# Optimization experiments

Measured on AMD Instinct MI355X. Metric: run time of the kernel, lower is better.

## Reference

```python
import jax, jax.numpy as jnp
import numpy as np


def setup_inputs() -> dict:
    key = jax.random.key(0)
    ks = jax.random.split(key, 6)
    S, B, E = 2048, 2, 1024
    scale = 1.0 / np.sqrt(E)
    return {
        "query": jax.random.normal(ks[0], (S, B, E), dtype=jnp.float32),
        "key": jax.random.normal(ks[1], (S, B, E), dtype=jnp.float32),
        "value": jax.random.normal(ks[2], (S, B, E), dtype=jnp.float32),
        "in_proj_w": jax.random.normal(ks[3], (3 * E, E), dtype=jnp.float32) * scale,
        "in_proj_b": jnp.zeros((3 * E,), dtype=jnp.float32),
        "out_proj_w": jax.random.normal(ks[4], (E, E), dtype=jnp.float32) * scale,
        "out_proj_b": jnp.zeros((E,), dtype=jnp.float32),
        "num_heads": 16,
        "block_size": 128,
    }


def reference(query, key, value, in_proj_w, in_proj_b, out_proj_w, out_proj_b,
              num_heads, block_size):
    # Shapes: query/key/value [S, B, E] (torch MHA default, batch_first=False)
    S, B, E = query.shape
    H = num_heads
    D = E // H

    wq, wk, wv = jnp.split(in_proj_w, 3, axis=0)   # each [E, E]
    bq, bk, bv = jnp.split(in_proj_b, 3, axis=0)   # each [E]

    def proj(x, w, b):
        # [S,B,E] @ [E,E]^T + b -> [B,H,S,D]
        y = x @ w.T + b
        return y.reshape(S, B, H, D).transpose(1, 2, 0, 3)

    q = proj(query, wq, bq) * (1.0 / np.sqrt(D))
    k = proj(key, wk, bk)
    v = proj(value, wv, bv)

    # Dense scores with banded mask: allowed iff i-block <= j <= i+block-1
    scores = jnp.einsum("bhsd,bhtd->bhst", q, k)  # [B,H,S,S]
    i = jnp.arange(S)[:, None]
    j = jnp.arange(S)[None, :]
    allowed = (j >= i - block_size) & (j < i + block_size)  # [S,S]
    neg_inf = jnp.asarray(-jnp.inf, dtype=scores.dtype)
    scores = jnp.where(allowed[None, None], scores, neg_inf)

    attn = jax.nn.softmax(scores, axis=-1)
    ctx = jnp.einsum("bhst,bhtd->bhsd", attn, v)           # [B,H,S,D]
    ctx = ctx.transpose(2, 0, 1, 3).reshape(S, B, E)       # [S,B,E]
    return ctx @ out_proj_w.T + out_proj_b
```

## Files before the change

### kernel.cpp

```cpp
#include <hip/hip_runtime.h>
#include <hip/hip_bf16.h>

#define S_LEN 2048
#define BATCH 2
#define EMB   1024
#define NHEAD 16
#define HDIM  64
#define WIN   128

typedef __attribute__((ext_vector_type(8))) short short8;
typedef __attribute__((ext_vector_type(4))) float floatx4;

__device__ __forceinline__ unsigned int pk2bf(float a, float b) {
    unsigned int ua = __builtin_bit_cast(unsigned int, a);
    unsigned int ub = __builtin_bit_cast(unsigned int, b);
    ua += 0x7fffu + ((ua >> 16) & 1u);
    ub += 0x7fffu + ((ub >> 16) & 1u);
    return (ua >> 16) | (ub & 0xffff0000u);
}
__device__ __forceinline__ unsigned short f2bf(float f) {
    unsigned int u = __builtin_bit_cast(unsigned int, f);
    u += 0x7fffu + ((u >> 16) & 1u);
    return (unsigned short)(u >> 16);
}

__device__ __forceinline__ void gl_lds16(const unsigned short* g, unsigned short* l) {
    __builtin_amdgcn_global_load_lds(
        (const __attribute__((address_space(1))) unsigned int*)g,
        (__attribute__((address_space(3))) unsigned int*)l,
        16, 0, 0);
}

#define QKV_UNITS 524288
#define WI_UNITS  393216
#define WO_UNITS  131072

__global__ __launch_bounds__(256)
void convert_kernel(const float* __restrict__ xq, const float* __restrict__ xk,
                    const float* __restrict__ xv, const float* __restrict__ wi,
                    const float* __restrict__ wo,
                    unsigned short* __restrict__ xqb, unsigned short* __restrict__ xkb,
                    unsigned short* __restrict__ xvb, unsigned short* __restrict__ wib,
                    unsigned short* __restrict__ wob)
{
    const size_t u = (size_t)blockIdx.x * 256 + threadIdx.x;
    const float* src;
    unsigned short* dst;
    size_t off;
    if (u < 3 * (size_t)QKV_UNITS) {
        const int which = (int)(u / QKV_UNITS);
        off = (u % QKV_UNITS) * 8;
        src = (which == 0) ? xq : (which == 1) ? xk : xv;
        dst = (which == 0) ? xqb : (which == 1) ? xkb : xvb;
    } else if (u < 3 * (size_t)QKV_UNITS + WI_UNITS) {
        off = (u - 3 * (size_t)QKV_UNITS) * 8;
        src = wi; dst = wib;
    } else {
        off = (u - (3 * (size_t)QKV_UNITS + WI_UNITS)) * 8;
        src = wo; dst = wob;
    }
    float4 a = *reinterpret_cast<const float4*>(src + off);
    float4 b = *reinterpret_cast<const float4*>(src + off + 4);
    uint4 p = {pk2bf(a.x, a.y), pk2bf(a.z, a.w), pk2bf(b.x, b.y), pk2bf(b.z, b.w)};
    *reinterpret_cast<uint4*>(dst + off) = p;
}

__global__ __launch_bounds__(256)
void qkv_gemm_kernel(const unsigned short* __restrict__ xqb,
                     const unsigned short* __restrict__ xkb,
                     const unsigned short* __restrict__ xvb,
                     const unsigned short* __restrict__ wib,
                     const float* __restrict__ bias,
                     unsigned short* __restrict__ qo,
                     unsigned short* __restrict__ ko,
                     unsigned short* __restrict__ vto)
{
    __shared__ unsigned short As[128 * 32];
    __shared__ unsigned short Bs[128 * 32];

    const int bid  = blockIdx.x;
    const int which = bid >> 8;
    const int bx   = (bid >> 5) & 7;
    const int by   = bid & 31;

    const unsigned short* A = (which == 0) ? xqb : (which == 1) ? xkb : xvb;
    const unsigned short* W = wib + (size_t)which * EMB * EMB;
    const float* bv = bias + which * EMB;
    const float scale = (which == 0) ? 0.125f : 1.0f;

    const int tid  = threadIdx.x;
    const int lane = tid & 63;
    const int wave = tid >> 6;
    const int quad = lane >> 4;
    const int c16  = lane & 15;
    const int wm   = (wave & 1) << 6;
    const int wn   = (wave >> 1) << 6;

    const int rowBase = by * 128;
    const int colBase = bx * 128;

    const int lrow = lane >> 2;
    const int lseg = (((lane & 3) ^ (lrow & 3)) << 3);

    floatx4 acc[4][4];
    #pragma unroll
    for (int i = 0; i < 4; ++i)
        #pragma unroll
        for (int j = 0; j < 4; ++j)
            acc[i][j] = (floatx4){0.f, 0.f, 0.f, 0.f};

    const int rxor = c16 & 3;

    for (int k0 = 0; k0 < EMB; k0 += 32) {
        __syncthreads();
        #pragma unroll
        for (int t = 0; t < 2; ++t) {
            const int c = wave * 2 + t;
            const int row = c * 16 + lrow;
            gl_lds16(A + (size_t)(rowBase + row) * EMB + k0 + lseg, &As[c * 512]);
            gl_lds16(W + (size_t)(colBase + row) * EMB + k0 + lseg, &Bs[c * 512]);
        }
        __syncthreads();

        const int soff = ((quad ^ rxor) << 3);
        short8 af[4], bf[4];
        #pragma unroll
        for (int mi = 0; mi < 4; ++mi)
            af[mi] = *reinterpret_cast<const short8*>(
                &As[(wm + mi * 16 + c16) * 32 + soff]);
        #pragma unroll
        for (int ni = 0; ni < 4; ++ni)
            bf[ni] = *reinterpret_cast<const short8*>(
                &Bs[(wn + ni * 16 + c16) * 32 + soff]);

        #pragma unroll
        for (int mi = 0; mi < 4; ++mi)
            #pragma unroll
            for (int ni = 0; ni < 4; ++ni)
                acc[mi][ni] = __builtin_amdgcn_mfma_f32_16x16x32_bf16(
                    af[mi], bf[ni], acc[mi][ni], 0, 0, 0);
    }

    #pragma unroll
    for (int ni = 0; ni < 4; ++ni) {
        const int n_full = colBase + wn + ni * 16 + c16;
        const float bb = bv[n_full];
        const int h = n_full >> 6;
        const int d = n_full & 63;
        #pragma unroll
        for (int mi = 0; mi < 4; ++mi) {
            #pragma unroll
            for (int r = 0; r < 4; ++r) {
                const int m_g = rowBase + wm + mi * 16 + quad * 4 + r;
                const int s   = m_g >> 1;
                const int b   = m_g & 1;
                const int bh  = b * NHEAD + h;
                const unsigned short val = f2bf((acc[mi][ni][r] + bb) * scale);
                if (which == 2)
                    vto[((size_t)bh * HDIM + d) * S_LEN + s] = val;
                else if (which == 0)
                    qo[((size_t)bh * S_LEN + s) * HDIM + d] = val;
                else
                    ko[((size_t)bh * S_LEN + s) * HDIM + d] = val;
            }
        }
    }
}

#define AT_STRIDE 72

__global__ __launch_bounds__(256)
void attn_mfma_kernel(const unsigned short* __restrict__ q,
                      const unsigned short* __restrict__ k,
                      const unsigned short* __restrict__ vt,
                      unsigned short* __restrict__ ctx)
{
    __shared__ unsigned short Qs[64 * AT_STRIDE];
    __shared__ unsigned short Ks[64 * AT_STRIDE];
    __shared__ unsigned short Vts[64 * AT_STRIDE];
    __shared__ unsigned short Ps[64 * AT_STRIDE];

    const int bid = blockIdx.x;
    const int bh  = bid & 31;
    const int s0  = (bid >> 5) * 64;
    const int tid = threadIdx.x;
    const int lane = tid & 63;
    const int wave = tid >> 6;
    const int quad = lane >> 4;
    const int c16  = lane & 15;

    const size_t base_qk = ((size_t)bh * S_LEN) * HDIM;
    const size_t base_vt = ((size_t)bh * HDIM) * S_LEN;

    const int srow = tid >> 2;
    const int sseg = (tid & 3) << 4;
    {
        const unsigned short* src = q + base_qk + (size_t)(s0 + srow) * HDIM + sseg;
        uint4 v0 = *reinterpret_cast<const uint4*>(src);
        uint4 v1 = *reinterpret_cast<const uint4*>(src + 8);
        *reinterpret_cast<uint4*>(&Qs[srow * AT_STRIDE + sseg])     = v0;
        *reinterpret_cast<uint4*>(&Qs[srow * AT_STRIDE + sseg + 8]) = v1;
    }

    float m_[4], l_[4];
    floatx4 ob[4];
    #pragma unroll
    for (int r = 0; r < 4; ++r) { m_[r] = -1.0e30f; l_[r] = 0.f; }
    #pragma unroll
    for (int dt = 0; dt < 4; ++dt) ob[dt] = (floatx4){0.f, 0.f, 0.f, 0.f};

    int c0 = s0 - 128; if (c0 < 0) c0 = 0;
    int c1 = s0 + 192; if (c1 > S_LEN) c1 = S_LEN;

    for (int cb = c0; cb < c1; cb += 64) {
        __syncthreads();
        {
            const unsigned short* ksrc = k + base_qk + (size_t)(cb + srow) * HDIM + sseg;
            const unsigned short* vsrc = vt + base_vt + (size_t)srow * S_LEN + cb + sseg;
            uint4 k0v = *reinterpret_cast<const uint4*>(ksrc);
            uint4 k1v = *reinterpret_cast<const uint4*>(ksrc + 8);
            uint4 v0v = *reinterpret_cast<const uint4*>(vsrc);
            uint4 v1v = *reinterpret_cast<const uint4*>(vsrc + 8);
            *reinterpret_cast<uint4*>(&Ks[srow * AT_STRIDE + sseg])      = k0v;
            *reinterpret_cast<uint4*>(&Ks[srow * AT_STRIDE + sseg + 8])  = k1v;
            *reinterpret_cast<uint4*>(&Vts[srow * AT_STRIDE + sseg])     = v0v;
            *reinterpret_cast<uint4*>(&Vts[srow * AT_STRIDE + sseg + 8]) = v1v;
        }
        __syncthreads();

        floatx4 sc[4];
        #pragma unroll
        for (int jt = 0; jt < 4; ++jt) sc[jt] = (floatx4){0.f, 0.f, 0.f, 0.f};
        {
            short8 af0 = *reinterpret_cast<const short8*>(
                &Qs[(wave * 16 + c16) * AT_STRIDE + quad * 8]);
            short8 af1 = *reinterpret_cast<const short8*>(
                &Qs[(wave * 16 + c16) * AT_STRIDE + 32 + quad * 8]);
            #pragma unroll
            for (int jt = 0; jt < 4; ++jt) {
                short8 bf0 = *reinterpret_cast<const short8*>(
                    &Ks[(jt * 16 + c16) * AT_STRIDE + quad * 8]);
                short8 bf1 = *reinterpret_cast<const short8*>(
                    &Ks[(jt * 16 + c16) * AT_STRIDE + 32 + quad * 8]);
                sc[jt] = __builtin_amdgcn_mfma_f32_16x16x32_bf16(af0, bf0, sc[jt], 0, 0, 0);
                sc[jt] = __builtin_amdgcn_mfma_f32_16x16x32_bf16(af1, bf1, sc[jt], 0, 0, 0);
            }
        }

        #pragma unroll
        for (int r = 0; r < 4; ++r) {
            const int qg = s0 + wave * 16 + quad * 4 + r;
            float rm = -3.0e38f;
            #pragma unroll
            for (int jt = 0; jt < 4; ++jt) {
                const int jg = cb + jt * 16 + c16;
                float x = sc[jt][r];
                if (jg < qg - WIN || jg >= qg + WIN) x = -3.0e38f;
                sc[jt][r] = x;
                rm = fmaxf(rm, x);
            }
            rm = fmaxf(rm, __shfl_xor(rm, 1));
            rm = fmaxf(rm, __shfl_xor(rm, 2));
            rm = fmaxf(rm, __shfl_xor(rm, 4));
            rm = fmaxf(rm, __shfl_xor(rm, 8));
            const float mn    = fmaxf(m_[r], rm);
            const float alpha = __expf(m_[r] - mn);
            float rs = 0.f;
            #pragma unroll
            for (int jt = 0; jt < 4; ++jt) {
                const float p = __expf(sc[jt][r] - mn);
                sc[jt][r] = p;
                rs += p;
            }
            rs += __shfl_xor(rs, 1);
            rs += __shfl_xor(rs, 2);
            rs += __shfl_xor(rs, 4);
            rs += __shfl_xor(rs, 8);
            l_[r] = l_[r] * alpha + rs;
            m_[r] = mn;
            #pragma unroll
            for (int dt = 0; dt < 4; ++dt) ob[dt][r] *= alpha;
        }

        #pragma unroll
        for (int jt = 0; jt < 4; ++jt)
            #pragma unroll
            for (int r = 0; r < 4; ++r)
                Ps[(wave * 16 + quad * 4 + r) * AT_STRIDE + jt * 16 + c16] =
                    f2bf(sc[jt][r]);

        {
            short8 pa0 = *reinterpret_cast<const short8*>(
                &Ps[(wave * 16 + c16) * AT_STRIDE + quad * 8]);
            short8 pa1 = *reinterpret_cast<const short8*>(
                &Ps[(wave * 16 + c16) * AT_STRIDE + 32 + quad * 8]);
            #pragma unroll
            for (int dt = 0; dt < 4; ++dt) {
                short8 bv0 = *reinterpret_cast<const short8*>(
                    &Vts[(dt * 16 + c16) * AT_STRIDE + quad * 8]);
                short8 bv1 = *reinterpret_cast<const short8*>(
                    &Vts[(dt * 16 + c16) * AT_STRIDE + 32 + quad * 8]);
                ob[dt] = __builtin_amdgcn_mfma_f32_16x16x32_bf16(pa0, bv0, ob[dt], 0, 0, 0);
                ob[dt] = __builtin_amdgcn_mfma_f32_16x16x32_bf16(pa1, bv1, ob[dt], 0, 0, 0);
            }
        }
    }

    const int b = bh >> 4;
    const int h = bh & 15;
    #pragma unroll
    for (int r = 0; r < 4; ++r) {
        const int sg  = s0 + wave * 16 + quad * 4 + r;
        const float inv = 1.0f / l_[r];
        #pragma unroll
        for (int dt = 0; dt < 4; ++dt) {
            const int d = dt * 16 + c16;
            ctx[((size_t)(sg * BATCH + b) << 10) + (h << 6) + d] = f2bf(ob[dt][r] * inv);
        }
    }
}

__global__ __launch_bounds__(256)
void out_gemm_kernel(const unsigned short* __restrict__ ctxb,
                     const unsigned short* __restrict__ wob,
                     const float* __restrict__ bias,
                     float* __restrict__ out)
{
    __shared__ unsigned short As[128 * 32];
    __shared__ unsigned short Bs[128 * 32];

    const int bid = blockIdx.x;
    const int bx  = bid >> 5;
    const int by  = bid & 31;

    const int tid  = threadIdx.x;
    const int lane = tid & 63;
    const int wave = tid >> 6;
    const int quad = lane >> 4;
    const int c16  = lane & 15;
    const int wm   = (wave & 1) << 6;
    const int wn   = (wave >> 1) << 6;

    const int rowBase = by * 128;
    const int colBase = bx * 128;

    const int lrow = lane >> 2;
    const int lseg = (((lane & 3) ^ (lrow & 3)) << 3);

    floatx4 acc[4][4];
    #pragma unroll
    for (int i = 0; i < 4; ++i)
        #pragma unroll
        for (int j = 0; j < 4; ++j)
            acc[i][j] = (floatx4){0.f, 0.f, 0.f, 0.f};

    const int rxor = c16 & 3;

    for (int k0 = 0; k0 < EMB; k0 += 32) {
        __syncthreads();
        #pragma unroll
        for (int t = 0; t < 2; ++t) {
            const int c = wave * 2 + t;
            const int row = c * 16 + lrow;
            gl_lds16(ctxb + (size_t)(rowBase + row) * EMB + k0 + lseg, &As[c * 512]);
            gl_lds16(wob  + (size_t)(colBase + row) * EMB + k0 + lseg, &Bs[c * 512]);
        }
        __syncthreads();

        const int soff = ((quad ^ rxor) << 3);
        short8 af[4], bf[4];
        #pragma unroll
        for (int mi = 0; mi < 4; ++mi)
            af[mi] = *reinterpret_cast<const short8*>(
                &As[(wm + mi * 16 + c16) * 32 + soff]);
        #pragma unroll
        for (int ni = 0; ni < 4; ++ni)
            bf[ni] = *reinterpret_cast<const short8*>(
                &Bs[(wn + ni * 16 + c16) * 32 + soff]);

        #pragma unroll
        for (int mi = 0; mi < 4; ++mi)
            #pragma unroll
            for (int ni = 0; ni < 4; ++ni)
                acc[mi][ni] = __builtin_amdgcn_mfma_f32_16x16x32_bf16(
                    af[mi], bf[ni], acc[mi][ni], 0, 0, 0);
    }

    #pragma unroll
    for (int ni = 0; ni < 4; ++ni) {
        const int n_full = colBase + wn + ni * 16 + c16;
        const float bb = bias[n_full];
        #pragma unroll
        for (int mi = 0; mi < 4; ++mi) {
            #pragma unroll
            for (int r = 0; r < 4; ++r) {
                const int m_g = rowBase + wm + mi * 16 + quad * 4 + r;
                out[(size_t)m_g * EMB + n_full] = acc[mi][ni][r] + bb;
            }
        }
    }
}

extern "C" void kernel_launch(void* const* d_in, const int* in_sizes, int n_in,
                              void* d_out, int out_size, void* d_ws, size_t ws_size,
                              hipStream_t stream) {
    const float* query = (const float*)d_in[0];
    const float* key   = (const float*)d_in[1];
    const float* value = (const float*)d_in[2];
    const float* in_w  = (const float*)d_in[3];
    const float* in_b  = (const float*)d_in[4];
    const float* out_w = (const float*)d_in[5];
    const float* out_b = (const float*)d_in[6];

    const size_t PLANE = (size_t)BATCH * NHEAD * S_LEN * HDIM;
    unsigned short* xqb = (unsigned short*)d_ws;
    unsigned short* xkb = xqb + PLANE;
    unsigned short* xvb = xkb + PLANE;
    unsigned short* wib = xvb + PLANE;
    unsigned short* wob = wib + (size_t)3 * EMB * EMB;
    unsigned short* qo  = wob + (size_t)EMB * EMB;
    unsigned short* ko  = qo + PLANE;
    unsigned short* vto = ko + PLANE;
    unsigned short* cw  = vto + PLANE;

    convert_kernel<<<8192, 256, 0, stream>>>(query, key, value, in_w, out_w,
                                             xqb, xkb, xvb, wib, wob);

    qkv_gemm_kernel<<<768, 256, 0, stream>>>(xqb, xkb, xvb, wib, in_b, qo, ko, vto);

    attn_mfma_kernel<<<1024, 256, 0, stream>>>(qo, ko, vto, cw);

    out_gemm_kernel<<<256, 256, 0, stream>>>(cw, wob, out_b, (float*)d_out);
}
```

Before: 201.5 us.

## Double-buffer GEMM LDS tiles, prefetch attention K/V, and stage V-transpose through LDS

Measured after the change: 214.7 us. 6.6% more time.

```diff
diff --git a/kernel.cpp b/kernel.cpp
--- a/kernel.cpp
+++ b/kernel.cpp
@@ -75,8 +75,8 @@
                      unsigned short* __restrict__ ko,
                      unsigned short* __restrict__ vto)
 {
-    __shared__ unsigned short As[128 * 32];
-    __shared__ unsigned short Bs[128 * 32];
+    __shared__ unsigned short As[2][128 * 32];
+    __shared__ unsigned short Bs[2][128 * 32];
 
     const int bid  = blockIdx.x;
     const int which = bid >> 8;
@@ -110,28 +110,37 @@
             acc[i][j] = (floatx4){0.f, 0.f, 0.f, 0.f};
 
     const int rxor = c16 & 3;
-
-    for (int k0 = 0; k0 < EMB; k0 += 32) {
-        __syncthreads();
-        #pragma unroll
-        for (int t = 0; t < 2; ++t) {
-            const int c = wave * 2 + t;
-            const int row = c * 16 + lrow;
-            gl_lds16(A + (size_t)(rowBase + row) * EMB + k0 + lseg, &As[c * 512]);
-            gl_lds16(W + (size_t)(colBase + row) * EMB + k0 + lseg, &Bs[c * 512]);
-        }
-        __syncthreads();
-
-        const int soff = ((quad ^ rxor) << 3);
+    const int soff = ((quad ^ rxor) << 3);
+
+#define STAGE_QKV(buf, kk)                                                        \
+    {                                                                             \
+        _Pragma("unroll")                                                         \
+        for (int t = 0; t < 2; ++t) {                                             \
+            const int c = wave * 2 + t;                                           \
+            const int row = c * 16 + lrow;                                        \
+            gl_lds16(A + (size_t)(rowBase + row) * EMB + (kk) + lseg,             \
+                     &As[buf][c * 512]);                                          \
+            gl_lds16(W + (size_t)(colBase + row) * EMB + (kk) + lseg,             \
+                     &Bs[buf][c * 512]);                                          \
+        }                                                                         \
+    }
+
+    STAGE_QKV(0, 0);
+    __syncthreads();
+
+    for (int it = 0; it < EMB / 32; ++it) {
+        const int cur = it & 1;
+        if (it + 1 < EMB / 32) STAGE_QKV(cur ^ 1, (it + 1) * 32);
+
         short8 af[4], bf[4];
         #pragma unroll
         for (int mi = 0; mi < 4; ++mi)
             af[mi] = *reinterpret_cast<const short8*>(
-                &As[(wm + mi * 16 + c16) * 32 + soff]);
+                &As[cur][(wm + mi * 16 + c16) * 32 + soff]);
         #pragma unroll
         for (int ni = 0; ni < 4; ++ni)
             bf[ni] = *reinterpret_cast<const short8*>(
-                &Bs[(wn + ni * 16 + c16) * 32 + soff]);
+                &Bs[cur][(wn + ni * 16 + c16) * 32 + soff]);
 
         #pragma unroll
         for (int mi = 0; mi < 4; ++mi)
@@ -139,30 +148,68 @@
             for (int ni = 0; ni < 4; ++ni)
                 acc[mi][ni] = __builtin_amdgcn_mfma_f32_16x16x32_bf16(
                     af[mi], bf[ni], acc[mi][ni], 0, 0, 0);
-    }
-
-    #pragma unroll
-    for (int ni = 0; ni < 4; ++ni) {
-        const int n_full = colBase + wn + ni * 16 + c16;
-        const float bb = bv[n_full];
+
+        __syncthreads();
+    }
+#undef STAGE_QKV
+
+    if (which != 2) {
+        #pragma unroll
+        for (int ni = 0; ni < 4; ++ni) {
+            const int n_full = colBase + wn + ni * 16 + c16;
+            const float bb = bv[n_full];
+            const int h = n_full >> 6;
+            const int d = n_full & 63;
+            #pragma unroll
+            for (int mi = 0; mi < 4; ++mi) {
+                #pragma unroll
+                for (int r = 0; r < 4; ++r) {
+                    const int m_g = rowBase + wm + mi * 16 + quad * 4 + r;
+                    const int s   = m_g >> 1;
+                    const int b   = m_g & 1;
+                    const int bh  = b * NHEAD + h;
+                    const unsigned short val = f2bf((acc[mi][ni][r] + bb) * scale);
+                    if (which == 0)
+                        qo[((size_t)bh * S_LEN + s) * HDIM + d] = val;
+                    else
+                        ko[((size_t)bh * S_LEN + s) * HDIM + d] = val;
+                }
+            }
+        }
+    } else {
+        unsigned short* Ts = (wn == 0) ? &As[0][0] : &Bs[0][0];
+        #pragma unroll
+        for (int ni = 0; ni < 4; ++ni) {
+            const int n_loc2 = ni * 16 + c16;
+            const int n_full = colBase + wn + n_loc2;
+            const float bb = bv[n_full];
+            const int k2 = (n_loc2 & 3) << 4;
+            #pragma unroll
+            for (int mi = 0; mi < 4; ++mi) {
+                #pragma unroll
+                for (int r = 0; r < 4; ++r) {
+                    const int m_local = wm + mi * 16 + quad * 4 + r;
+                    const int lin = (m_local & 1) * 64 + (m_local >> 1);
+                    Ts[n_loc2 * 128 + (lin ^ k2)] = f2bf(acc[mi][ni][r] + bb);
+                }
+            }
+        }
+        __syncthreads();
+        const int nl = tid & 127;
+        const int b  = tid >> 7;
+        const int n_loc2 = nl & 63;
+        const unsigned short* Tsrc = (nl < 64) ? &As[0][0] : &Bs[0][0];
+        const int k2 = (n_loc2 & 3) << 4;
+        const int n_full = colBase + nl;
         const int h = n_full >> 6;
         const int d = n_full & 63;
-        #pragma unroll
-        for (int mi = 0; mi < 4; ++mi) {
-            #pragma unroll
-            for (int r = 0; r < 4; ++r) {
-                const int m_g = rowBase + wm + mi * 16 + quad * 4 + r;
-                const int s   = m_g >> 1;
-                const int b   = m_g & 1;
-                const int bh  = b * NHEAD + h;
-                const unsigned short val = f2bf((acc[mi][ni][r] + bb) * scale);
-                if (which == 2)
-                    vto[((size_t)bh * HDIM + d) * S_LEN + s] = val;
-                else if (which == 0)
-                    qo[((size_t)bh * S_LEN + s) * HDIM + d] = val;
-                else
-                    ko[((size_t)bh * S_LEN + s) * HDIM + d] = val;
-            }
+        const int bh = b * NHEAD + h;
+        unsigned short* dst = vto + ((size_t)bh * HDIM + d) * S_LEN + (rowBase >> 1);
+        #pragma unroll
+        for (int g = 0; g < 8; ++g) {
+            const uint4 vv = *reinterpret_cast<const uint4*>(
+                &Tsrc[n_loc2 * 128 + ((b * 64 + g * 8) ^ k2)]);
+            *reinterpret_cast<uint4*>(dst + g * 8) = vv;
         }
     }
 }
@@ -212,21 +259,27 @@
     int c0 = s0 - 128; if (c0 < 0) c0 = 0;
     int c1 = s0 + 192; if (c1 > S_LEN) c1 = S_LEN;
 
+    uint4 k0v, k1v, v0v, v1v;
+#define LOADKV(CB)                                                                \
+    {                                                                             \
+        const unsigned short* ksrc = k + base_qk + (size_t)((CB) + srow) * HDIM + sseg; \
+        const unsigned short* vsrc = vt + base_vt + (size_t)srow * S_LEN + (CB) + sseg; \
+        k0v = *reinterpret_cast<const uint4*>(ksrc);                              \
+        k1v = *reinterpret_cast<const uint4*>(ksrc + 8);                          \
+        v0v = *reinterpret_cast<const uint4*>(vsrc);                              \
+        v1v = *reinterpret_cast<const uint4*>(vsrc + 8);                          \
+    }
+
+    LOADKV(c0);
+
     for (int cb = c0; cb < c1; cb += 64) {
         __syncthreads();
-        {
-            const unsigned short* ksrc = k + base_qk + (size_t)(cb + srow) * HDIM + sseg;
-            const unsigned short* vsrc = vt + base_vt + (size_t)srow * S_LEN + cb + sseg;
-            uint4 k0v = *reinterpret_cast<const uint4*>(ksrc);
-            uint4 k1v = *reinterpret_cast<const uint4*>(ksrc + 8);
-            uint4 v0v = *reinterpret_cast<const uint4*>(vsrc);
-            uint4 v1v = *reinterpret_cast<const uint4*>(vsrc + 8);
-            *reinterpret_cast<uint4*>(&Ks[srow * AT_STRIDE + sseg])      = k0v;
-            *reinterpret_cast<uint4*>(&Ks[srow * AT_STRIDE + sseg + 8])  = k1v;
-            *reinterpret_cast<uint4*>(&Vts[srow * AT_STRIDE + sseg])     = v0v;
-            *reinterpret_cast<uint4*>(&Vts[srow * AT_STRIDE + sseg + 8]) = v1v;
-        }
+        *reinterpret_cast<uint4*>(&Ks[srow * AT_STRIDE + sseg])      = k0v;
+        *reinterpret_cast<uint4*>(&Ks[srow * AT_STRIDE + sseg + 8])  = k1v;
+        *reinterpret_cast<uint4*>(&Vts[srow * AT_STRIDE + sseg])     = v0v;
+        *reinterpret_cast<uint4*>(&Vts[srow * AT_STRIDE + sseg + 8]) = v1v;
         __syncthreads();
+        if (cb + 64 < c1) LOADKV(cb + 64);
 
         floatx4 sc[4];
         #pragma unroll
@@ -305,6 +358,7 @@
             }
         }
     }
+#undef LOADKV
 
     const int b = bh >> 4;
     const int h = bh & 15;
@@ -326,8 +380,8 @@
                      const float* __restrict__ bias,
                      float* __restrict__ out)
 {
-    __shared__ unsigned short As[128 * 32];
-    __shared__ unsigned short Bs[128 * 32];
+    __shared__ unsigned short As[2][128 * 32];
+    __shared__ unsigned short Bs[2][128 * 32];
 
     const int bid = blockIdx.x;
     const int bx  = bid >> 5;
@@ -355,28 +409,37 @@
             acc[i][j] = (floatx4){0.f, 0.f, 0.f, 0.f};
 
     const int rxor = c16 & 3;
-
-    for (int k0 = 0; k0 < EMB; k0 += 32) {
-        __syncthreads();
-        #pragma unroll
-        for (int t = 0; t < 2; ++t) {
-            const int c = wave * 2 + t;
-            const int row = c * 16 + lrow;
-            gl_lds16(ctxb + (size_t)(rowBase + row) * EMB + k0 + lseg, &As[c * 512]);
-            gl_lds16(wob  + (size_t)(colBase + row) * EMB + k0 + lseg, &Bs[c * 512]);
-        }
-        __syncthreads();
-
-        const int soff = ((quad ^ rxor) << 3);
+    const int soff = ((quad ^ rxor) << 3);
+
+#define STAGE_OUT(buf, kk)                                                        \
+    {                                                                             \
+        _Pragma("unroll")                                                         \
+        for (int t = 0; t < 2; ++t) {                                             \
+            const int c = wave * 2 + t;                                           \
+            const int row = c * 16 + lrow;                                        \
+            gl_lds16(ctxb + (size_t)(rowBase + row) * EMB + (kk) + lseg,          \
+                     &As[buf][c * 512]);                                          \
+            gl_lds16(wob  + (size_t)(colBase + row) * EMB + (kk) + lseg,          \
+                     &Bs[buf][c * 512]);                                          \
+        }                                                                         \
+    }
+
+    STAGE_OUT(0, 0);
+    __syncthreads();
+
+    for (int it = 0; it < EMB / 32; ++it) {
+        const int cur = it & 1;
+        if (it + 1 < EMB / 32) STAGE_OUT(cur ^ 1, (it + 1) * 32);
+
         short8 af[4], bf[4];
         #pragma unroll
         for (int mi = 0; mi < 4; ++mi)
             af[mi] = *reinterpret_cast<const short8*>(
-                &As[(wm + mi * 16 + c16) * 32 + soff]);
+                &As[cur][(wm + mi * 16 + c16) * 32 + soff]);
         #pragma unroll
         for (int ni = 0; ni < 4; ++ni)
             bf[ni] = *reinterpret_cast<const short8*>(
-                &Bs[(wn + ni * 16 + c16) * 32 + soff]);
+                &Bs[cur][(wn + ni * 16 + c16) * 32 + soff]);
 
         #pragma unroll
         for (int mi = 0; mi < 4; ++mi)
@@ -384,7 +447,10 @@
             for (int ni = 0; ni < 4; ++ni)
                 acc[mi][ni] = __builtin_amdgcn_mfma_f32_16x16x32_bf16(
                     af[mi], bf[ni], acc[mi][ni], 0, 0, 0);
-    }
+
+        __syncthreads();
+    }
+#undef STAGE_OUT
 
     #pragma unroll
     for (int ni = 0; ni < 4; ++ni) {
```
